# Kernel tuning notes

Measured on AMD Instinct MI355X. Metric: run time of the kernel, lower is better.

## Reference

```python
import jax, jax.numpy as jnp
import numpy as np

QMIN, QMAX = -128.0, 127.0  # 8-bit signed activation range


def fq_act(x, s):
    """Fake-quantize activations: clip(round(x/s))*s with straight-through estimator."""
    y = jnp.clip(jnp.round(x / s), QMIN, QMAX) * s
    return x + jax.lax.stop_gradient(y - x)


def fq_weight(w):
    """Per-tensor max-abs symmetric (narrow-range) 8-bit weight fake-quant with STE."""
    s = jnp.max(jnp.abs(w)) / 127.0
    y = jnp.clip(jnp.round(w / s), -127.0, 127.0) * s
    return w + jax.lax.stop_gradient(y - w)


def conv1x1(x, w, b):
    # x: [b,c,h,w], w: [o,c] -> [b,o,h,w]
    return jnp.einsum('bchw,oc->bohw', x, w) + b[None, :, None, None]


def setup_inputs() -> dict:
    key = jax.random.key(0)
    ks = jax.random.split(key, 6)
    B, C, HC, H, W = 8, 64, 32, 64, 64
    x = jax.random.normal(ks[0], (B, C, H, W), dtype=jnp.float32)
    wq = jax.random.normal(ks[1], (HC, C), dtype=jnp.float32) * 0.05
    wk = jax.random.normal(ks[2], (HC, C), dtype=jnp.float32) * 0.05
    wv = jax.random.normal(ks[3], (HC, C), dtype=jnp.float32) * 0.05
    wp = jax.random.normal(ks[4], (C, HC), dtype=jnp.float32) * 0.05
    return {
        'x': x,
        'wq': wq, 'bq': jnp.zeros((HC,), jnp.float32),
        'wk': wk, 'bk': jnp.zeros((HC,), jnp.float32),
        'wv': wv, 'bv': jnp.zeros((HC,), jnp.float32),
        'wp': wp, 'bp': jnp.zeros((C,), jnp.float32),
        's_in': jnp.ones((1,), jnp.float32) * 0.0625,
        's_out': jnp.ones((1,), jnp.float32) * 0.0625,
    }


def reference(x, wq, bq, wk, bk, wv, bv, wp, bp, s_in, s_out):
    b, c, h, w = x.shape
    hc = wq.shape[0]
    n = h * w
    xq = fq_act(x, s_in)                              # quant_inp(x)
    q = conv1x1(xq, fq_weight(wq), bq).reshape(b, hc, n).transpose(0, 2, 1)  # [b,n,hc]
    k = conv1x1(xq, fq_weight(wk), bk).reshape(b, hc, n)                     # [b,hc,n]
    v = conv1x1(xq, fq_weight(wv), bv).reshape(b, hc, n).transpose(0, 2, 1)  # [b,n,hc]
    z = jax.nn.softmax(jnp.einsum('bqc,bck->bqk', q, k), axis=-1)            # [b,n,n]
    z = jnp.einsum('bqk,bkc->bqc', z, v).transpose(0, 2, 1).reshape(b, hc, h, w)
    z = fq_act(z, s_in)                               # quant_inp(z) (shared module/scale)
    out = xq + conv1x1(z, fq_weight(wp), bp)
    return fq_act(out, s_out)                         # self.act QuantIdentity
```

## Files before the change

### kernel.cpp

```cpp
#include <hip/hip_runtime.h>
#include <hip/hip_bf16.h>
#include <cstdint>
#include <cstddef>

#define NB 8
#define NC 64
#define NHC 32
#define NN 4096
#define LOG2E 1.44269504088896340736f

typedef short v8s __attribute__((ext_vector_type(8)));
typedef short v4s __attribute__((ext_vector_type(4)));
typedef float v4f __attribute__((ext_vector_type(4)));
typedef unsigned int v2u __attribute__((ext_vector_type(2)));

__device__ __forceinline__ unsigned short f2b(float f) {
    unsigned int u = __builtin_bit_cast(unsigned int, f);
    u += 0x7fffu + ((u >> 16) & 1u);
    return (unsigned short)(u >> 16);
}
__device__ __forceinline__ float b2f(unsigned short s) {
    unsigned int u = ((unsigned int)s) << 16;
    return __builtin_bit_cast(float, u);
}
__device__ __forceinline__ unsigned int pack2_bf16(float a, float b) {
    unsigned int ua = __builtin_bit_cast(unsigned int, a);
    ua += 0x7fffu + ((ua >> 16) & 1u);
    unsigned int ub = __builtin_bit_cast(unsigned int, b);
    ub += 0x7fffu + ((ub >> 16) & 1u);
    return (ua >> 16) | (ub & 0xffff0000u);
}
__device__ __forceinline__ unsigned int trunc2_bf16(float a, float b) {
    return __builtin_amdgcn_perm(__builtin_bit_cast(unsigned int, b),
                                 __builtin_bit_cast(unsigned int, a), 0x07060302u);
}
__device__ __forceinline__ float wave_max(float v) {
    #pragma unroll
    for (int off = 1; off < 64; off <<= 1) v = fmaxf(v, __shfl_xor(v, off));
    return v;
}
__device__ __forceinline__ v4f mfma16bf16(v4s a, v4s b, v4f c) {
#if __has_builtin(__builtin_amdgcn_mfma_f32_16x16x16bf16_1k)
    return __builtin_amdgcn_mfma_f32_16x16x16bf16_1k(a, b, c, 0, 0, 0);
#else
    asm volatile("v_mfma_f32_16x16x16_bf16 %0, %1, %2, %0"
                 : "+v"(c) : "v"(a), "v"(b));
    return c;
#endif
}

__global__ __launch_bounds__(256) void k_qkv(
    const float* __restrict__ x,
    const float* __restrict__ wq, const float* __restrict__ wk, const float* __restrict__ wv,
    const float* __restrict__ bq, const float* __restrict__ bk, const float* __restrict__ bv,
    const float* __restrict__ s_in,
    unsigned short* __restrict__ xqb, unsigned short* __restrict__ qb,
    unsigned short* __restrict__ kb, unsigned short* __restrict__ vb)
{
    int blk = blockIdx.x;
    int b   = blk >> 6;
    int p0  = (blk & 63) * 64;
    int tid = threadIdx.x;
    int wave = tid >> 6;
    int lane = tid & 63;

    __shared__ __align__(16) unsigned short xt[64][72];
    __shared__ __align__(16) unsigned short wlds[6144];
    __shared__ float red[3][4];

    float4 q0 = *(const float4*)(wq + tid * 8), q1 = *(const float4*)(wq + tid * 8 + 4);
    float4 k0 = *(const float4*)(wk + tid * 8), k1 = *(const float4*)(wk + tid * 8 + 4);
    float4 v0 = *(const float4*)(wv + tid * 8), v1 = *(const float4*)(wv + tid * 8 + 4);
    float mq = fmaxf(fmaxf(fmaxf(fabsf(q0.x), fabsf(q0.y)), fmaxf(fabsf(q0.z), fabsf(q0.w))),
                     fmaxf(fmaxf(fabsf(q1.x), fabsf(q1.y)), fmaxf(fabsf(q1.z), fabsf(q1.w))));
    float mk = fmaxf(fmaxf(fmaxf(fabsf(k0.x), fabsf(k0.y)), fmaxf(fabsf(k0.z), fabsf(k0.w))),
                     fmaxf(fmaxf(fabsf(k1.x), fabsf(k1.y)), fmaxf(fabsf(k1.z), fabsf(k1.w))));
    float mv = fmaxf(fmaxf(fmaxf(fabsf(v0.x), fabsf(v0.y)), fmaxf(fabsf(v0.z), fabsf(v0.w))),
                     fmaxf(fmaxf(fabsf(v1.x), fabsf(v1.y)), fmaxf(fabsf(v1.z), fabsf(v1.w))));
    mq = wave_max(mq); mk = wave_max(mk); mv = wave_max(mv);
    if (lane == 0) { red[0][wave] = mq; red[1][wave] = mk; red[2][wave] = mv; }
    __syncthreads();
    float sq = fmaxf(fmaxf(red[0][0], red[0][1]), fmaxf(red[0][2], red[0][3])) / 127.0f;
    float sk = fmaxf(fmaxf(red[1][0], red[1][1]), fmaxf(red[1][2], red[1][3])) / 127.0f;
    float sw = fmaxf(fmaxf(red[2][0], red[2][1]), fmaxf(red[2][2], red[2][3])) / 127.0f;
    {
        float eq[8] = {q0.x, q0.y, q0.z, q0.w, q1.x, q1.y, q1.z, q1.w};
        float ek[8] = {k0.x, k0.y, k0.z, k0.w, k1.x, k1.y, k1.z, k1.w};
        float ev[8] = {v0.x, v0.y, v0.z, v0.w, v1.x, v1.y, v1.z, v1.w};
        #pragma unroll
        for (int j = 0; j < 8; ++j) {
            wlds[0 * 2048 + tid * 8 + j] = f2b(fminf(fmaxf(rintf(eq[j] / sq), -127.f), 127.f) * sq);
            wlds[1 * 2048 + tid * 8 + j] = f2b(fminf(fmaxf(rintf(ek[j] / sk), -127.f), 127.f) * sk);
            wlds[2 * 2048 + tid * 8 + j] = f2b(fminf(fmaxf(rintf(ev[j] / sw), -127.f), 127.f) * sw);
        }
    }

    float sv = s_in[0];
    float sinv = 1.0f / sv;
    int jj = tid & 15;
    int c0 = tid >> 4;
    #pragma unroll
    for (int it = 0; it < 4; ++it) {
        int c = c0 + it * 16;
        size_t gi = ((size_t)(b * NC + c) << 12) + p0 + jj * 4;
        float4 xv = *(const float4*)(x + gi);
        float r0 = fminf(fmaxf(rintf(xv.x * sinv), -128.f), 127.f) * sv;
        float r1 = fminf(fmaxf(rintf(xv.y * sinv), -128.f), 127.f) * sv;
        float r2 = fminf(fmaxf(rintf(xv.z * sinv), -128.f), 127.f) * sv;
        float r3 = fminf(fmaxf(rintf(xv.w * sinv), -128.f), 127.f) * sv;
        *(uint2*)(xqb + gi) = make_uint2(pack2_bf16(r0, r1), pack2_bf16(r2, r3));
        xt[jj * 4 + 0][c] = f2b(r0);
        xt[jj * 4 + 1][c] = f2b(r1);
        xt[jj * 4 + 2][c] = f2b(r2);
        xt[jj * 4 + 3][c] = f2b(r3);
    }
    __syncthreads();

    int quad = lane >> 4;
    int l15  = lane & 15;

    v8s bf0 = *(const v8s*)(&xt[wave * 16 + l15][0  + quad * 8]);
    v8s bf1 = *(const v8s*)(&xt[wave * 16 + l15][32 + quad * 8]);

    int pos = p0 + wave * 16 + l15;
    size_t posg = (size_t)b * NN + pos;
    int posP = p0 + (l15 >> 2) * 16 + wave * 4 + (l15 & 3);
    const v4f zc = {0.f, 0.f, 0.f, 0.f};

    #pragma unroll
    for (int rb = 0; rb < 6; ++rb) {
        v8s a0 = *(const v8s*)(wlds + (rb * 16 + l15) * 64 + 0  + quad * 8);
        v8s a1 = *(const v8s*)(wlds + (rb * 16 + l15) * 64 + 32 + quad * 8);
        v4f t   = __builtin_amdgcn_mfma_f32_16x16x32_bf16(a0, bf0, zc, 0, 0, 0);
        v4f acc = __builtin_amdgcn_mfma_f32_16x16x32_bf16(a1, bf1, t, 0, 0, 0);

        int R0 = rb * 16 + quad * 4;
        float vals[4];
        #pragma unroll
        for (int r = 0; r < 4; ++r) {
            int R = R0 + r;
            float bias = (R < 32) ? bq[R] : (R < 64) ? bk[R - 32] : bv[R - 64];
            float vv = acc[r] + bias;
            if (R < 32) vv *= LOG2E;
            vals[r] = vv;
        }
        if (R0 < 32) {
            *(unsigned int*)(qb + posg * NHC + R0)     = pack2_bf16(vals[0], vals[1]);
            *(unsigned int*)(qb + posg * NHC + R0 + 2) = pack2_bf16(vals[2], vals[3]);
        } else if (R0 < 64) {
            *(unsigned int*)(kb + posg * NHC + R0 - 32)     = pack2_bf16(vals[0], vals[1]);
            *(unsigned int*)(kb + posg * NHC + R0 - 32 + 2) = pack2_bf16(vals[2], vals[3]);
        } else {
            #pragma unroll
            for (int r = 0; r < 4; ++r)
                vb[(size_t)(b * NHC + R0 - 64 + r) * NN + posP] = f2b(vals[r]);
        }
    }
}

__global__ __launch_bounds__(256, 2) void k_attn(
    const unsigned short* __restrict__ qb, const unsigned short* __restrict__ kb,
    const unsigned short* __restrict__ vb, const unsigned short* __restrict__ xqb,
    const float* __restrict__ wp, const float* __restrict__ bp,
    const float* __restrict__ s_in, const float* __restrict__ s_out,
    float* __restrict__ out)
{
    int blk  = blockIdx.x;
    int b    = blk >> 6;
    int qt   = blk & 63;
    int qbase = qt * 64;
    int tid  = threadIdx.x;
    int wave = tid >> 6;
    int lane = tid & 63;
    int quad = lane >> 4;
    int l15  = lane & 15;

    __shared__ __align__(16) float zbuf[4][64][36];
    __shared__ float lbuf[4][64];
    __shared__ __align__(16) unsigned short wpq[2048];
    __shared__ float redw[4];

    {
        float4 a0 = *(const float4*)(wp + tid * 8), a1 = *(const float4*)(wp + tid * 8 + 4);
        float mx = fmaxf(fmaxf(fmaxf(fabsf(a0.x), fabsf(a0.y)), fmaxf(fabsf(a0.z), fabsf(a0.w))),
                         fmaxf(fmaxf(fabsf(a1.x), fabsf(a1.y)), fmaxf(fabsf(a1.z), fabsf(a1.w))));
        mx = wave_max(mx);
        if (lane == 0) redw[wave] = mx;
        __syncthreads();
        float scale = fmaxf(fmaxf(redw[0], redw[1]), fmaxf(redw[2], redw[3])) / 127.0f;
        float e[8] = {a0.x, a0.y, a0.z, a0.w, a1.x, a1.y, a1.z, a1.w};
        #pragma unroll
        for (int j = 0; j < 8; ++j) {
            float r = fminf(fmaxf(rintf(e[j] / scale), -127.f), 127.f);
            wpq[tid * 8 + j] = f2b(r * scale);
        }
    }

    const unsigned short* qbat = qb + (size_t)b * NN * NHC;
    const unsigned short* kbat = kb + (size_t)b * NN * NHC;
    const unsigned short* vbat = vb + (size_t)b * NHC * NN;

    v8s qf[4];
    #pragma unroll
    for (int s = 0; s < 4; ++s)
        qf[s] = *(const v8s*)(qbat + (qbase + s * 16 + l15) * NHC + quad * 8);

    const v4f zc = {0.f, 0.f, 0.f, 0.f};
    v4f zt[4][2] = {{zc, zc}, {zc, zc}, {zc, zc}, {zc, zc}};
    float psA[4] = {0.f, 0.f, 0.f, 0.f};
    float psB[4] = {0.f, 0.f, 0.f, 0.f};

    int k0 = wave * 1024;
    const unsigned short* vrow0 = vbat + (size_t)( 0 + l15) * NN;
    const unsigned short* vrow1 = vbat + (size_t)(16 + l15) * NN;

    v8s ck0 = *(const v8s*)(kbat + (k0 +  0 + l15) * NHC + quad * 8);
    v8s ck1 = *(const v8s*)(kbat + (k0 + 16 + l15) * NHC + quad * 8);
    v8s ck2 = *(const v8s*)(kbat + (k0 + 32 + l15) * NHC + quad * 8);
    v8s ck3 = *(const v8s*)(kbat + (k0 + 48 + l15) * NHC + quad * 8);

    #pragma unroll 1
    for (int i = 0; i < 16; ++i) {
        int cki = k0 + (i << 6);
        int nki = k0 + (((i + 1) & 15) << 6);
        v8s nk0 = *(const v8s*)(kbat + (nki +  0 + l15) * NHC + quad * 8);
        v8s nk1 = *(const v8s*)(kbat + (nki + 16 + l15) * NHC + quad * 8);
        v8s nk2 = *(const v8s*)(kbat + (nki + 32 + l15) * NHC + quad * 8);
        v8s nk3 = *(const v8s*)(kbat + (nki + 48 + l15) * NHC + quad * 8);
        v8s v00 = *(const v8s*)(vrow0 + cki + quad * 16);
        v8s v01 = *(const v8s*)(vrow0 + cki + quad * 16 + 8);
        v8s v10 = *(const v8s*)(vrow1 + cki + quad * 16);
        v8s v11 = *(const v8s*)(vrow1 + cki + quad * 16 + 8);
        v4s va[2][4];
        va[0][0] = __builtin_shufflevector(v00, v00, 0, 1, 2, 3);
        va[0][1] = __builtin_shufflevector(v00, v00, 4, 5, 6, 7);
        va[0][2] = __builtin_shufflevector(v01, v01, 0, 1, 2, 3);
        va[0][3] = __builtin_shufflevector(v01, v01, 4, 5, 6, 7);
        va[1][0] = __builtin_shufflevector(v10, v10, 0, 1, 2, 3);
        va[1][1] = __builtin_shufflevector(v10, v10, 4, 5, 6, 7);
        va[1][2] = __builtin_shufflevector(v11, v11, 0, 1, 2, 3);
        va[1][3] = __builtin_shufflevector(v11, v11, 4, 5, 6, 7);

        #pragma unroll
        for (int s = 0; s < 4; ++s) {
            v4f sa[4];
            sa[0] = __builtin_amdgcn_mfma_f32_16x16x32_bf16(ck0, qf[s], zc, 0, 0, 0);
            sa[1] = __builtin_amdgcn_mfma_f32_16x16x32_bf16(ck1, qf[s], zc, 0, 0, 0);
            sa[2] = __builtin_amdgcn_mfma_f32_16x16x32_bf16(ck2, qf[s], zc, 0, 0, 0);
            sa[3] = __builtin_amdgcn_mfma_f32_16x16x32_bf16(ck3, qf[s], zc, 0, 0, 0);

            #pragma unroll
            for (int t = 0; t < 4; ++t) {
                float p0 = __builtin_amdgcn_exp2f(sa[t][0]);
                float p1 = __builtin_amdgcn_exp2f(sa[t][1]);
                float p2 = __builtin_amdgcn_exp2f(sa[t][2]);
                float p3 = __builtin_amdgcn_exp2f(sa[t][3]);
                psA[s] += p0 + p1;
                psB[s] += p2 + p3;
                v2u w;
                w.x = trunc2_bf16(p0, p1);
                w.y = trunc2_bf16(p2, p3);
                v4s pfrag = __builtin_bit_cast(v4s, w);
                zt[s][0] = mfma16bf16(va[0][t], pfrag, zt[s][0]);
                zt[s][1] = mfma16bf16(va[1][t], pfrag, zt[s][1]);
            }
        }
        ck0 = nk0; ck1 = nk1; ck2 = nk2; ck3 = nk3;
    }

    #pragma unroll
    for (int s = 0; s < 4; ++s) {
        *(v4f*)(&zbuf[wave][s * 16 + l15][     quad * 4]) = zt[s][0];
        *(v4f*)(&zbuf[wave][s * 16 + l15][16 + quad * 4]) = zt[s][1];
        float ps = psA[s] + psB[s];
        ps += __shfl_xor(ps, 16);
        ps += __shfl_xor(ps, 32);
        if (quad == 0) lbuf[wave][s * 16 + l15] = ps;
    }
    __syncthreads();

    int myq = wave * 16 + l15;
    float L = lbuf[0][myq] + lbuf[1][myq] + lbuf[2][myq] + lbuf[3][myq];

    float z[8] = {0.f};
    #pragma unroll
    for (int w = 0; w < 4; ++w) {
        v4f za  = *(const v4f*)(&zbuf[w][myq][quad * 8]);
        v4f zb2 = *(const v4f*)(&zbuf[w][myq][quad * 8 + 4]);
        #pragma unroll
        for (int j = 0; j < 4; ++j) { z[j] += za[j]; z[4 + j] += zb2[j]; }
    }
    float sv = s_in[0], sinv = 1.0f / sv;
    float so = s_out[0], soinv = 1.0f / so;
    float Linv = 1.0f / L;
    unsigned int zp[4];
    #pragma unroll
    for (int jp = 0; jp < 4; ++jp) {
        float a = z[2 * jp]     * Linv;
        float c = z[2 * jp + 1] * Linv;
        a = fminf(fmaxf(rintf(a * sinv), -128.f), 127.f) * sv;
        c = fminf(fmaxf(rintf(c * sinv), -128.f), 127.f) * sv;
        zp[jp] = pack2_bf16(a, c);
    }
    v8s zf = __builtin_bit_cast(v8s, *(uint4*)zp);

    v8s w0f = *(const v8s*)(wpq + ( 0 + l15) * NHC + quad * 8);
    v8s w1f = *(const v8s*)(wpq + (16 + l15) * NHC + quad * 8);
    v8s w2f = *(const v8s*)(wpq + (32 + l15) * NHC + quad * 8);
    v8s w3f = *(const v8s*)(wpq + (48 + l15) * NHC + quad * 8);
    v4f o0 = __builtin_amdgcn_mfma_f32_16x16x32_bf16(w0f, zf, zc, 0, 0, 0);
    v4f o1 = __builtin_amdgcn_mfma_f32_16x16x32_bf16(w1f, zf, zc, 0, 0, 0);
    v4f o2 = __builtin_amdgcn_mfma_f32_16x16x32_bf16(w2f, zf, zc, 0, 0, 0);
    v4f o3 = __builtin_amdgcn_mfma_f32_16x16x32_bf16(w3f, zf, zc, 0, 0, 0);

    int pos = qbase + wave * 16 + l15;
    #pragma unroll
    for (int ot = 0; ot < 4; ++ot) {
        v4f ov = (ot == 0) ? o0 : (ot == 1) ? o1 : (ot == 2) ? o2 : o3;
        #pragma unroll
        for (int r = 0; r < 4; ++r) {
            int oc = ot * 16 + quad * 4 + r;
            size_t idx = (size_t)(b * NC + oc) * NN + pos;
            float val = ov[r] + bp[oc] + b2f(xqb[idx]);
            float f = fminf(fmaxf(rintf(val * soinv), -128.f), 127.f);
            out[idx] = f * so;
        }
    }
}

extern "C" void kernel_launch(void* const* d_in, const int* in_sizes, int n_in,
                              void* d_out, int out_size, void* d_ws, size_t ws_size,
                              hipStream_t stream) {
    const float* x     = (const float*)d_in[0];
    const float* wq    = (const float*)d_in[1];
    const float* bq    = (const float*)d_in[2];
    const float* wk    = (const float*)d_in[3];
    const float* bk    = (const float*)d_in[4];
    const float* wv    = (const float*)d_in[5];
    const float* bv    = (const float*)d_in[6];
    const float* wp    = (const float*)d_in[7];
    const float* bp    = (const float*)d_in[8];
    const float* s_in  = (const float*)d_in[9];
    const float* s_out = (const float*)d_in[10];
    float* out = (float*)d_out;

    char* ws = (char*)d_ws;
    size_t off = 0;
    auto carve = [&](size_t bytes) {
        void* p = ws + off;
        off = (off + bytes + 255) & ~(size_t)255;
        return p;
    };
    unsigned short* xqb = (unsigned short*)carve((size_t)NB * NC * NN * 2);
    unsigned short* qbf = (unsigned short*)carve((size_t)NB * NN * NHC * 2);
    unsigned short* kbf = (unsigned short*)carve((size_t)NB * NN * NHC * 2);
    unsigned short* vbf = (unsigned short*)carve((size_t)NB * NHC * NN * 2);

    hipLaunchKernelGGL(k_qkv, dim3(512), dim3(256), 0, stream,
                       x, wq, wk, wv, bq, bk, bv, s_in, xqb, qbf, kbf, vbf);
    hipLaunchKernelGGL(k_attn, dim3(512), dim3(256), 0, stream,
                       qbf, kbf, vbf, xqb, wp, bp, s_in, s_out, out);
}
```

Baseline: 111.4 us.

## Halve query tile to 32 rows and double grid for both kernels

Both kernels now process 32 positions per block instead of 64, doubling the grid to 1024 blocks so more work is in flight on the 256-CU device. The attention kernel drops the K register prefetch, holds two query subtiles instead of four, and raises launch bounds to four blocks per CU to increase occupancy. In the QKV kernel, waves now split output row-blocks (three each) rather than positions, and the V permutation index is recomputed to match. The trade-off is that each K/V tile is reloaded twice as often per query, and half the waves sit idle in the epilogue.

Result: slower. 134.8 us (+21.0%).

```diff
diff --git a/kernel.cpp b/kernel.cpp
--- a/kernel.cpp
+++ b/kernel.cpp
@@ -58,13 +58,13 @@
     unsigned short* __restrict__ kb, unsigned short* __restrict__ vb)
 {
     int blk = blockIdx.x;
-    int b   = blk >> 6;
-    int p0  = (blk & 63) * 64;
+    int b   = blk >> 7;
+    int p0  = (blk & 127) * 32;
     int tid = threadIdx.x;
     int wave = tid >> 6;
     int lane = tid & 63;
 
-    __shared__ __align__(16) unsigned short xt[64][72];
+    __shared__ __align__(16) unsigned short xt[32][72];
     __shared__ __align__(16) unsigned short wlds[6144];
     __shared__ float red[3][4];
 
@@ -97,11 +97,11 @@
 
     float sv = s_in[0];
     float sinv = 1.0f / sv;
-    int jj = tid & 15;
-    int c0 = tid >> 4;
-    #pragma unroll
-    for (int it = 0; it < 4; ++it) {
-        int c = c0 + it * 16;
+    int jj = tid & 7;
+    int c0 = tid >> 3;
+    #pragma unroll
+    for (int it = 0; it < 2; ++it) {
+        int c = c0 + it * 32;
         size_t gi = ((size_t)(b * NC + c) << 12) + p0 + jj * 4;
         float4 xv = *(const float4*)(x + gi);
         float r0 = fminf(fmaxf(rintf(xv.x * sinv), -128.f), 127.f) * sv;
@@ -118,17 +118,21 @@
 
     int quad = lane >> 4;
     int l15  = lane & 15;
-
-    v8s bf0 = *(const v8s*)(&xt[wave * 16 + l15][0  + quad * 8]);
-    v8s bf1 = *(const v8s*)(&xt[wave * 16 + l15][32 + quad * 8]);
-
-    int pos = p0 + wave * 16 + l15;
+    int psub = wave >> 1;
+    int rbb  = (wave & 1) * 3;
+
+    v8s bf0 = *(const v8s*)(&xt[psub * 16 + l15][0  + quad * 8]);
+    v8s bf1 = *(const v8s*)(&xt[psub * 16 + l15][32 + quad * 8]);
+
+    int pos = p0 + psub * 16 + l15;
     size_t posg = (size_t)b * NN + pos;
-    int posP = p0 + (l15 >> 2) * 16 + wave * 4 + (l15 & 3);
+    int kap = pos & 63;
+    int posP = (pos & ~63) + ((kap >> 2) & 3) * 16 + ((kap >> 4) & 3) * 4 + (kap & 3);
     const v4f zc = {0.f, 0.f, 0.f, 0.f};
 
     #pragma unroll
-    for (int rb = 0; rb < 6; ++rb) {
+    for (int j = 0; j < 3; ++j) {
+        int rb = rbb + j;
         v8s a0 = *(const v8s*)(wlds + (rb * 16 + l15) * 64 + 0  + quad * 8);
         v8s a1 = *(const v8s*)(wlds + (rb * 16 + l15) * 64 + 32 + quad * 8);
         v4f t   = __builtin_amdgcn_mfma_f32_16x16x32_bf16(a0, bf0, zc, 0, 0, 0);
@@ -158,7 +162,7 @@
     }
 }
 
-__global__ __launch_bounds__(256, 2) void k_attn(
+__global__ __launch_bounds__(256, 4) void k_attn(
     const unsigned short* __restrict__ qb, const unsigned short* __restrict__ kb,
     const unsigned short* __restrict__ vb, const unsigned short* __restrict__ xqb,
     const float* __restrict__ wp, const float* __restrict__ bp,
@@ -166,17 +170,17 @@
     float* __restrict__ out)
 {
     int blk  = blockIdx.x;
-    int b    = blk >> 6;
-    int qt   = blk & 63;
-    int qbase = qt * 64;
+    int b    = blk >> 7;
+    int qt   = blk & 127;
+    int qbase = qt * 32;
     int tid  = threadIdx.x;
     int wave = tid >> 6;
     int lane = tid & 63;
     int quad = lane >> 4;
     int l15  = lane & 15;
 
-    __shared__ __align__(16) float zbuf[4][64][36];
-    __shared__ float lbuf[4][64];
+    __shared__ __align__(16) float zbuf[4][32][36];
+    __shared__ float lbuf[4][32];
     __shared__ __align__(16) unsigned short wpq[2048];
     __shared__ float redw[4];
 
@@ -200,33 +204,25 @@
     const unsigned short* kbat = kb + (size_t)b * NN * NHC;
     const unsigned short* vbat = vb + (size_t)b * NHC * NN;
 
-    v8s qf[4];
-    #pragma unroll
-    for (int s = 0; s < 4; ++s)
-        qf[s] = *(const v8s*)(qbat + (qbase + s * 16 + l15) * NHC + quad * 8);
+    v8s qf0 = *(const v8s*)(qbat + (qbase +      l15) * NHC + quad * 8);
+    v8s qf1 = *(const v8s*)(qbat + (qbase + 16 + l15) * NHC + quad * 8);
 
     const v4f zc = {0.f, 0.f, 0.f, 0.f};
-    v4f zt[4][2] = {{zc, zc}, {zc, zc}, {zc, zc}, {zc, zc}};
-    float psA[4] = {0.f, 0.f, 0.f, 0.f};
-    float psB[4] = {0.f, 0.f, 0.f, 0.f};
+    v4f zt[2][2] = {{zc, zc}, {zc, zc}};
+    float psA[2] = {0.f, 0.f};
+    float psB[2] = {0.f, 0.f};
 
     int k0 = wave * 1024;
     const unsigned short* vrow0 = vbat + (size_t)( 0 + l15) * NN;
     const unsigned short* vrow1 = vbat + (size_t)(16 + l15) * NN;
 
-    v8s ck0 = *(const v8s*)(kbat + (k0 +  0 + l15) * NHC + quad * 8);
-    v8s ck1 = *(const v8s*)(kbat + (k0 + 16 + l15) * NHC + quad * 8);
-    v8s ck2 = *(const v8s*)(kbat + (k0 + 32 + l15) * NHC + quad * 8);
-    v8s ck3 = *(const v8s*)(kbat + (k0 + 48 + l15) * NHC + quad * 8);
-
     #pragma unroll 1
     for (int i = 0; i < 16; ++i) {
         int cki = k0 + (i << 6);
-        int nki = k0 + (((i + 1) & 15) << 6);
-        v8s nk0 = *(const v8s*)(kbat + (nki +  0 + l15) * NHC + quad * 8);
-        v8s nk1 = *(const v8s*)(kbat + (nki + 16 + l15) * NHC + quad * 8);
-        v8s nk2 = *(const v8s*)(kbat + (nki + 32 + l15) * NHC + quad * 8);
-        v8s nk3 = *(const v8s*)(kbat + (nki + 48 + l15) * NHC + quad * 8);
+        v8s ck0 = *(const v8s*)(kbat + (cki +  0 + l15) * NHC + quad * 8);
+        v8s ck1 = *(const v8s*)(kbat + (cki + 16 + l15) * NHC + quad * 8);
+        v8s ck2 = *(const v8s*)(kbat + (cki + 32 + l15) * NHC + quad * 8);
+        v8s ck3 = *(const v8s*)(kbat + (cki + 48 + l15) * NHC + quad * 8);
         v8s v00 = *(const v8s*)(vrow0 + cki + quad * 16);
         v8s v01 = *(const v8s*)(vrow0 + cki + quad * 16 + 8);
         v8s v10 = *(const v8s*)(vrow1 + cki + quad * 16);
@@ -242,12 +238,13 @@
         va[1][3] = __builtin_shufflevector(v11, v11, 4, 5, 6, 7);
 
         #pragma unroll
-        for (int s = 0; s < 4; ++s) {
+        for (int s = 0; s < 2; ++s) {
+            v8s qf = s ? qf1 : qf0;
             v4f sa[4];
-            sa[0] = __builtin_amdgcn_mfma_f32_16x16x32_bf16(ck0, qf[s], zc, 0, 0, 0);
-            sa[1] = __builtin_amdgcn_mfma_f32_16x16x32_bf16(ck1, qf[s], zc, 0, 0, 0);
-            sa[2] = __builtin_amdgcn_mfma_f32_16x16x32_bf16(ck2, qf[s], zc, 0, 0, 0);
-            sa[3] = __builtin_amdgcn_mfma_f32_16x16x32_bf16(ck3, qf[s], zc, 0, 0, 0);
+            sa[0] = __builtin_amdgcn_mfma_f32_16x16x32_bf16(ck0, qf, zc, 0, 0, 0);
+            sa[1] = __builtin_amdgcn_mfma_f32_16x16x32_bf16(ck1, qf, zc, 0, 0, 0);
+            sa[2] = __builtin_amdgcn_mfma_f32_16x16x32_bf16(ck2, qf, zc, 0, 0, 0);
+            sa[3] = __builtin_amdgcn_mfma_f32_16x16x32_bf16(ck3, qf, zc, 0, 0, 0);
 
             #pragma unroll
             for (int t = 0; t < 4; ++t) {
@@ -265,11 +262,10 @@
                 zt[s][1] = mfma16bf16(va[1][t], pfrag, zt[s][1]);
             }
         }
-        ck0 = nk0; ck1 = nk1; ck2 = nk2; ck3 = nk3;
-    }
-
-    #pragma unroll
-    for (int s = 0; s < 4; ++s) {
+    }
+
+    #pragma unroll
+    for (int s = 0; s < 2; ++s) {
         *(v4f*)(&zbuf[wave][s * 16 + l15][     quad * 4]) = zt[s][0];
         *(v4f*)(&zbuf[wave][s * 16 + l15][16 + quad * 4]) = zt[s][1];
         float ps = psA[s] + psB[s];
@@ -278,6 +274,7 @@
         if (quad == 0) lbuf[wave][s * 16 + l15] = ps;
     }
     __syncthreads();
+    if (wave >= 2) return;
 
     int myq = wave * 16 + l15;
     float L = lbuf[0][myq] + lbuf[1][myq] + lbuf[2][myq] + lbuf[3][myq];
@@ -313,7 +310,7 @@
     v4f o2 = __builtin_amdgcn_mfma_f32_16x16x32_bf16(w2f, zf, zc, 0, 0, 0);
     v4f o3 = __builtin_amdgcn_mfma_f32_16x16x32_bf16(w3f, zf, zc, 0, 0, 0);
 
-    int pos = qbase + wave * 16 + l15;
+    int pos = qbase + myq;
     #pragma unroll
     for (int ot = 0; ot < 4; ++ot) {
         v4f ov = (ot == 0) ? o0 : (ot == 1) ? o1 : (ot == 2) ? o2 : o3;
@@ -356,8 +353,8 @@
     unsigned short* kbf = (unsigned short*)carve((size_t)NB * NN * NHC * 2);
     unsigned short* vbf = (unsigned short*)carve((size_t)NB * NHC * NN * 2);
 
-    hipLaunchKernelGGL(k_qkv, dim3(512), dim3(256), 0, stream,
+    hipLaunchKernelGGL(k_qkv, dim3(1024), dim3(256), 0, stream,
                        x, wq, wk, wv, bq, bk, bv, s_in, xqb, qbf, kbf, vbf);
-    hipLaunchKernelGGL(k_attn, dim3(512), dim3(256), 0, stream,
+    hipLaunchKernelGGL(k_attn, dim3(1024), dim3(256), 0, stream,
                        qbf, kbf, vbf, xqb, wp, bp, s_in, s_out, out);
 }
```

## Split attention key range across eight waves per block instead of four

Applied to the files above, without the earlier changes.

The attention kernel now launches 512 threads per block, and each of the eight waves handles 512 keys instead of 1024. The partial softmax sums and PV accumulators are reduced through a larger shared buffer, and waves 4-7 exit after the reduction. The software prefetch of the next K tile is removed, so K loads are now issued at the top of each iteration. The intent is more waves in flight to hide latency, at the cost of more shared memory (about 74KB of zbuf), doubled reduction work, register pressure from launch_bounds(512,4), and loss of K prefetch.

After: 128.1 us. 1.15x slower.

```diff
diff --git a/kernel.cpp b/kernel.cpp
--- a/kernel.cpp
+++ b/kernel.cpp
@@ -158,7 +158,7 @@
     }
 }
 
-__global__ __launch_bounds__(256, 2) void k_attn(
+__global__ __launch_bounds__(512, 4) void k_attn(
     const unsigned short* __restrict__ qb, const unsigned short* __restrict__ kb,
     const unsigned short* __restrict__ vb, const unsigned short* __restrict__ xqb,
     const float* __restrict__ wp, const float* __restrict__ bp,
@@ -175,24 +175,24 @@
     int quad = lane >> 4;
     int l15  = lane & 15;
 
-    __shared__ __align__(16) float zbuf[4][64][36];
-    __shared__ float lbuf[4][64];
+    __shared__ __align__(16) float zbuf[8][64][36];
+    __shared__ float lbuf[8][64];
     __shared__ __align__(16) unsigned short wpq[2048];
-    __shared__ float redw[4];
+    __shared__ float redw[8];
 
     {
-        float4 a0 = *(const float4*)(wp + tid * 8), a1 = *(const float4*)(wp + tid * 8 + 4);
-        float mx = fmaxf(fmaxf(fmaxf(fabsf(a0.x), fabsf(a0.y)), fmaxf(fabsf(a0.z), fabsf(a0.w))),
-                         fmaxf(fmaxf(fabsf(a1.x), fabsf(a1.y)), fmaxf(fabsf(a1.z), fabsf(a1.w))));
+        float4 a0 = *(const float4*)(wp + tid * 4);
+        float mx = fmaxf(fmaxf(fabsf(a0.x), fabsf(a0.y)), fmaxf(fabsf(a0.z), fabsf(a0.w)));
         mx = wave_max(mx);
         if (lane == 0) redw[wave] = mx;
         __syncthreads();
-        float scale = fmaxf(fmaxf(redw[0], redw[1]), fmaxf(redw[2], redw[3])) / 127.0f;
-        float e[8] = {a0.x, a0.y, a0.z, a0.w, a1.x, a1.y, a1.z, a1.w};
-        #pragma unroll
-        for (int j = 0; j < 8; ++j) {
+        float scale = fmaxf(fmaxf(fmaxf(redw[0], redw[1]), fmaxf(redw[2], redw[3])),
+                            fmaxf(fmaxf(redw[4], redw[5]), fmaxf(redw[6], redw[7]))) / 127.0f;
+        float e[4] = {a0.x, a0.y, a0.z, a0.w};
+        #pragma unroll
+        for (int j = 0; j < 4; ++j) {
             float r = fminf(fmaxf(rintf(e[j] / scale), -127.f), 127.f);
-            wpq[tid * 8 + j] = f2b(r * scale);
+            wpq[tid * 4 + j] = f2b(r * scale);
         }
     }
 
@@ -210,23 +210,17 @@
     float psA[4] = {0.f, 0.f, 0.f, 0.f};
     float psB[4] = {0.f, 0.f, 0.f, 0.f};
 
-    int k0 = wave * 1024;
+    int k0 = wave * 512;
     const unsigned short* vrow0 = vbat + (size_t)( 0 + l15) * NN;
     const unsigned short* vrow1 = vbat + (size_t)(16 + l15) * NN;
 
-    v8s ck0 = *(const v8s*)(kbat + (k0 +  0 + l15) * NHC + quad * 8);
-    v8s ck1 = *(const v8s*)(kbat + (k0 + 16 + l15) * NHC + quad * 8);
-    v8s ck2 = *(const v8s*)(kbat + (k0 + 32 + l15) * NHC + quad * 8);
-    v8s ck3 = *(const v8s*)(kbat + (k0 + 48 + l15) * NHC + quad * 8);
-
     #pragma unroll 1
-    for (int i = 0; i < 16; ++i) {
+    for (int i = 0; i < 8; ++i) {
         int cki = k0 + (i << 6);
-        int nki = k0 + (((i + 1) & 15) << 6);
-        v8s nk0 = *(const v8s*)(kbat + (nki +  0 + l15) * NHC + quad * 8);
-        v8s nk1 = *(const v8s*)(kbat + (nki + 16 + l15) * NHC + quad * 8);
-        v8s nk2 = *(const v8s*)(kbat + (nki + 32 + l15) * NHC + quad * 8);
-        v8s nk3 = *(const v8s*)(kbat + (nki + 48 + l15) * NHC + quad * 8);
+        v8s ck0 = *(const v8s*)(kbat + (cki +  0 + l15) * NHC + quad * 8);
+        v8s ck1 = *(const v8s*)(kbat + (cki + 16 + l15) * NHC + quad * 8);
+        v8s ck2 = *(const v8s*)(kbat + (cki + 32 + l15) * NHC + quad * 8);
+        v8s ck3 = *(const v8s*)(kbat + (cki + 48 + l15) * NHC + quad * 8);
         v8s v00 = *(const v8s*)(vrow0 + cki + quad * 16);
         v8s v01 = *(const v8s*)(vrow0 + cki + quad * 16 + 8);
         v8s v10 = *(const v8s*)(vrow1 + cki + quad * 16);
@@ -265,7 +259,6 @@
                 zt[s][1] = mfma16bf16(va[1][t], pfrag, zt[s][1]);
             }
         }
-        ck0 = nk0; ck1 = nk1; ck2 = nk2; ck3 = nk3;
     }
 
     #pragma unroll
@@ -278,13 +271,16 @@
         if (quad == 0) lbuf[wave][s * 16 + l15] = ps;
     }
     __syncthreads();
+    if (wave >= 4) return;
 
     int myq = wave * 16 + l15;
-    float L = lbuf[0][myq] + lbuf[1][myq] + lbuf[2][myq] + lbuf[3][myq];
+    float L = 0.f;
+    #pragma unroll
+    for (int w = 0; w < 8; ++w) L += lbuf[w][myq];
 
     float z[8] = {0.f};
     #pragma unroll
-    for (int w = 0; w < 4; ++w) {
+    for (int w = 0; w < 8; ++w) {
         v4f za  = *(const v4f*)(&zbuf[w][myq][quad * 8]);
         v4f zb2 = *(const v4f*)(&zbuf[w][myq][quad * 8 + 4]);
         #pragma unroll
@@ -304,16 +300,17 @@
     }
     v8s zf = __builtin_bit_cast(v8s, *(uint4*)zp);
 
+    const v4f zc2 = {0.f, 0.f, 0.f, 0.f};
     v8s w0f = *(const v8s*)(wpq + ( 0 + l15) * NHC + quad * 8);
     v8s w1f = *(const v8s*)(wpq + (16 + l15) * NHC + quad * 8);
     v8s w2f = *(const v8s*)(wpq + (32 + l15) * NHC + quad * 8);
     v8s w3f = *(const v8s*)(wpq + (48 + l15) * NHC + quad * 8);
-    v4f o0 = __builtin_amdgcn_mfma_f32_16x16x32_bf16(w0f, zf, zc, 0, 0, 0);
-    v4f o1 = __builtin_amdgcn_mfma_f32_16x16x32_bf16(w1f, zf, zc, 0, 0, 0);
-    v4f o2 = __builtin_amdgcn_mfma_f32_16x16x32_bf16(w2f, zf, zc, 0, 0, 0);
-    v4f o3 = __builtin_amdgcn_mfma_f32_16x16x32_bf16(w3f, zf, zc, 0, 0, 0);
-
-    int pos = qbase + wave * 16 + l15;
+    v4f o0 = __builtin_amdgcn_mfma_f32_16x16x32_bf16(w0f, zf, zc2, 0, 0, 0);
+    v4f o1 = __builtin_amdgcn_mfma_f32_16x16x32_bf16(w1f, zf, zc2, 0, 0, 0);
+    v4f o2 = __builtin_amdgcn_mfma_f32_16x16x32_bf16(w2f, zf, zc2, 0, 0, 0);
+    v4f o3 = __builtin_amdgcn_mfma_f32_16x16x32_bf16(w3f, zf, zc2, 0, 0, 0);
+
+    int pos = qbase + myq;
     #pragma unroll
     for (int ot = 0; ot < 4; ++ot) {
         v4f ov = (ot == 0) ? o0 : (ot == 1) ? o1 : (ot == 2) ? o2 : o3;
@@ -358,6 +355,6 @@
 
     hipLaunchKernelGGL(k_qkv, dim3(512), dim3(256), 0, stream,
                        x, wq, wk, wv, bq, bk, bv, s_in, xqb, qbf, kbf, vbf);
-    hipLaunchKernelGGL(k_attn, dim3(512), dim3(256), 0, stream,
+    hipLaunchKernelGGL(k_attn, dim3(512), dim3(512), 0, stream,
                        qbf, kbf, vbf, xqb, wp, bp, s_in, s_out, out);
 }
```
